# Kernel tuning notes

Measured on AMD Instinct MI355X. Metric: run time of the kernel, lower is better.

## Reference

```python
import jax, jax.numpy as jnp
import numpy as np

B, S, D_IN, D_OUT = 4, 2048, 1024, 1024

def setup_inputs() -> dict:
    key = jax.random.key(0)
    kx, kq, kk, kv = jax.random.split(key, 4)
    x = jax.random.normal(kx, (B, S, D_IN), dtype=jnp.float32)
    # torch nn.Linear weight is [d_out, d_in]; we store the transposed [d_in, d_out]
    # so y = x @ W, scaled like default init to keep magnitudes sane.
    scale = 1.0 / np.sqrt(D_IN)
    Wq = jax.random.normal(kq, (D_IN, D_OUT), dtype=jnp.float32) * scale
    Wk = jax.random.normal(kk, (D_IN, D_OUT), dtype=jnp.float32) * scale
    Wv = jax.random.normal(kv, (D_IN, D_OUT), dtype=jnp.float32) * scale
    return {"x": x, "Wq": Wq, "Wk": Wk, "Wv": Wv}

def reference(x, Wq, Wk, Wv):
    b, n, _ = x.shape
    q = jnp.einsum('bnd,de->bne', x, Wq)   # [B,S,D_OUT]
    k = jnp.einsum('bnd,de->bne', x, Wk)
    v = jnp.einsum('bnd,de->bne', x, Wv)
    scores = jnp.einsum('bqe,bke->bqk', q, k) / jnp.sqrt(jnp.float32(k.shape[-1]))
    causal = jnp.triu(jnp.ones((n, n), dtype=bool), k=1)  # True above diagonal -> masked
    scores = jnp.where(causal[None, :, :], -jnp.inf, scores)
    weights = jax.nn.softmax(scores, axis=-1)
    # dropout p=0.0 (deterministic baseline) -> identity
    context = jnp.einsum('bqk,bke->bqe', weights, v)
    return context
```

## Files before the change

kernel.cpp:

```cpp
#include <hip/hip_runtime.h>
#include <hip/hip_bf16.h>

#define BB 4
#define SS 2048
#define DD 1024

typedef __attribute__((ext_vector_type(8))) short bf16x8;
typedef __attribute__((ext_vector_type(4))) float f32x4;

__device__ __forceinline__ ushort f2bf(float f) {
  unsigned u = __float_as_uint(f);
  unsigned r = (u + 0x7fffu + ((u >> 16) & 1u)) >> 16;
  return (ushort)r;
}

__device__ __forceinline__ void gload_lds16(const void* g, void* l) {
  __builtin_amdgcn_global_load_lds(
      (const __attribute__((address_space(1))) void*)g,
      (__attribute__((address_space(3))) void*)l, 16, 0, 0);
}

__global__ __launch_bounds__(256) void cast_x_kernel(const float* __restrict__ x,
                                                     ushort* __restrict__ xb) {
  const int i = blockIdx.x * 256 + threadIdx.x;
  const float4 a = ((const float4*)x)[2 * i];
  const float4 b = ((const float4*)x)[2 * i + 1];
  ushort4 o0, o1;
  o0.x = f2bf(a.x); o0.y = f2bf(a.y); o0.z = f2bf(a.z); o0.w = f2bf(a.w);
  o1.x = f2bf(b.x); o1.y = f2bf(b.y); o1.z = f2bf(b.z); o1.w = f2bf(b.w);
  ((ushort4*)xb)[2 * i] = o0;
  ((ushort4*)xb)[2 * i + 1] = o1;
}

__global__ __launch_bounds__(256) void cast_transpose_w(const float* __restrict__ W0,
                                                        const float* __restrict__ W1,
                                                        const float* __restrict__ W2,
                                                        ushort* __restrict__ Wt) {
  const float* W = blockIdx.z == 0 ? W0 : (blockIdx.z == 1 ? W1 : W2);
  ushort* O = Wt + (size_t)blockIdx.z * DD * DD;
  __shared__ ushort t[32][33];
  const int n0 = blockIdx.x * 32, k0 = blockIdx.y * 32;
  const int tx = threadIdx.x, ty = threadIdx.y;
#pragma unroll
  for (int j = 0; j < 4; j++) {
    int k = k0 + ty + j * 8;
    t[ty + j * 8][tx] = f2bf(W[(size_t)k * DD + n0 + tx]);
  }
  __syncthreads();
#pragma unroll
  for (int j = 0; j < 4; j++) {
    int n = ty + j * 8;
    O[(size_t)(n0 + n) * DD + k0 + tx] = t[tx][n];
  }
}

template <int BM, int BN, int GMODE, bool EXPMASK, bool KCLIP, bool DIVL, bool OUT_BF16>
__global__ __launch_bounds__(512) void gemm8(const ushort* __restrict__ A, int lda, size_t strA,
                                             const ushort* __restrict__ Bt, int ldb, size_t strB,
                                             void* __restrict__ C, int ldc, size_t strC, int K,
                                             int NBX) {
  constexpr int LA = BM / 64;
  constexpr int LB = BN / 64;
  constexpr int FM = BM / 32;
  constexpr int FN = BN / 64;
  int nb, mb, bz;
  if (GMODE == 2) {
    constexpr int NMB = SS / BM;
    constexpr int T = NMB * (NMB + 1) / 2;
    int flat = blockIdx.x + T * blockIdx.z;
    flat = (flat & 7) * ((T * BB) >> 3) + (flat >> 3);
    bz = flat / T;
    int i = flat % T;
    mb = (int)((sqrtf(8.f * i + 1.f) - 1.f) * 0.5f);
    while ((mb + 1) * (mb + 2) / 2 <= i) ++mb;
    while (mb * (mb + 1) / 2 > i) --mb;
    nb = i - mb * (mb + 1) / 2;
  } else if (GMODE == 1) {
    const int nwg = gridDim.x;
    int L = (blockIdx.x & 7) * (nwg >> 3) + (blockIdx.x >> 3);
    nb = L % NBX;
    mb = L / NBX;
    bz = 0;
  } else if (GMODE == 3) {
    int L = (blockIdx.x & 7) * 64 + (blockIdx.x >> 3);
    nb = L & 7;
    int G = L >> 3;
    bz = G & 3;
    int h = G >> 2;
    mb = (h & 1) ? (15 - (h >> 1)) : (h >> 1);
  } else {
    nb = blockIdx.x; mb = blockIdx.y; bz = blockIdx.z;
  }
  const ushort* Ab = A + (size_t)bz * strA;
  const ushort* Bb = Bt + (size_t)bz * strB;

  __shared__ ushort lds[2][(BM + BN) * 64];

  const int tid = threadIdx.x;
  const int lane = tid & 63;
  const int wid = tid >> 6;
  const int wr = wid >> 2, wc = wid & 3;
  const int fr = lane & 15, qq = lane >> 4;
  const int sx = (fr & 7) << 4;

  int kEnd = KCLIP ? (mb + 1) * BM : K;
  if (kEnd > K) kEnd = K;
  const int NT = kEnd >> 6;

  auto stage = [&](int kt, int buf) {
    ushort* As = &lds[buf][0];
    ushort* Bs = &lds[buf][BM * 64];
    const ushort* ga = Ab + (size_t)mb * BM * lda + kt * 64;
    const ushort* gb = Bb + (size_t)nb * BN * ldb + kt * 64;
#pragma unroll
    for (int j = 0; j < LA; j++) {
      int D = (j * 512 + tid) * 16;
      int r = D >> 7;
      int cb = (D & 127) ^ ((r & 7) << 4);
      gload_lds16(ga + (size_t)r * lda + (cb >> 1), (char*)As + D);
    }
#pragma unroll
    for (int j = 0; j < LB; j++) {
      int D = (j * 512 + tid) * 16;
      int r = D >> 7;
      int cb = (D & 127) ^ ((r & 7) << 4);
      gload_lds16(gb + (size_t)r * ldb + (cb >> 1), (char*)Bs + D);
    }
  };

  stage(0, 0);
  if (NT > 1) stage(1, 1);

  f32x4 acc[FM][FN] = {};
  float lsum[FM];
#pragma unroll
  for (int i = 0; i < FM; i++) lsum[i] = 0.f;

  for (int kt = 0; kt < NT; ++kt) {
    const int cur = kt & 1;
    if (kt < NT - 1) {
      if constexpr (LA + LB == 6) asm volatile("s_waitcnt vmcnt(6)" ::: "memory");
      else if constexpr (LA + LB == 4) asm volatile("s_waitcnt vmcnt(4)" ::: "memory");
      else asm volatile("s_waitcnt vmcnt(0)" ::: "memory");
    } else {
      asm volatile("s_waitcnt vmcnt(0)" ::: "memory");
    }
    __builtin_amdgcn_s_barrier();
    __builtin_amdgcn_sched_barrier(0);

    const char* As = (const char*)&lds[cur][0];
    const char* Bs = (const char*)&lds[cur][BM * 64];
    __builtin_amdgcn_s_setprio(1);
#pragma unroll
    for (int ks = 0; ks < 2; ++ks) {
      const int kb = ks * 64 + qq * 16;
      bf16x8 a[FM], b[FN];
#pragma unroll
      for (int i = 0; i < FM; i++) {
        int r = wr * (BM / 2) + i * 16 + fr;
        a[i] = *(const bf16x8*)(As + r * 128 + (kb ^ sx));
      }
#pragma unroll
      for (int j = 0; j < FN; j++) {
        int r = wc * (BN / 4) + j * 16 + fr;
        b[j] = *(const bf16x8*)(Bs + r * 128 + (kb ^ sx));
      }
      if (DIVL && wc == 0) {
#pragma unroll
        for (int i = 0; i < FM; i++)
#pragma unroll
          for (int e = 0; e < 8; e++)
            lsum[i] += __uint_as_float((unsigned)(unsigned short)a[i][e] << 16);
      }
#pragma unroll
      for (int i = 0; i < FM; i++)
#pragma unroll
        for (int j = 0; j < FN; j++)
          acc[i][j] = __builtin_amdgcn_mfma_f32_16x16x32_bf16(a[i], b[j], acc[i][j], 0, 0, 0);
    }
    __builtin_amdgcn_s_setprio(0);
    __builtin_amdgcn_s_barrier();
    __builtin_amdgcn_sched_barrier(0);
    if (kt + 2 < NT) stage(kt + 2, cur);
  }

  __shared__ float lds_l[2][BM / 2];
  if (DIVL) {
    if (wc == 0) {
#pragma unroll
      for (int i = 0; i < FM; i++) {
        lsum[i] += __shfl_xor(lsum[i], 16);
        lsum[i] += __shfl_xor(lsum[i], 32);
      }
      if (qq == 0) {
#pragma unroll
        for (int i = 0; i < FM; i++) lds_l[wr][i * 16 + fr] = lsum[i];
      }
    }
    __syncthreads();
  }

  const int col0 = nb * BN + wc * (BN / 4) + fr;
  const int row00 = mb * BM + wr * (BM / 2) + qq * 4;
  if (OUT_BF16) {
    ushort* Cb = (ushort*)C + (size_t)bz * strC;
#pragma unroll
    for (int i = 0; i < FM; i++)
#pragma unroll
      for (int rr = 0; rr < 4; rr++) {
        const int row = row00 + i * 16 + rr;
        size_t ro = (size_t)row * ldc;
#pragma unroll
        for (int j = 0; j < FN; j++) {
          float v = acc[i][j][rr];
          if (EXPMASK) {
            v = __expf(v * 0.03125f);
            if (col0 + j * 16 > row) v = 0.f;
          }
          Cb[ro + col0 + j * 16] = f2bf(v);
        }
      }
  } else {
    float* Cb = (float*)C + (size_t)bz * strC;
#pragma unroll
    for (int i = 0; i < FM; i++)
#pragma unroll
      for (int rr = 0; rr < 4; rr++) {
        size_t ro = (size_t)(row00 + i * 16 + rr) * ldc;
        float invl = 1.f;
        if (DIVL) invl = 1.f / lds_l[wr][i * 16 + qq * 4 + rr];
#pragma unroll
        for (int j = 0; j < FN; j++) Cb[ro + col0 + j * 16] = acc[i][j][rr] * invl;
      }
  }
}

extern "C" void kernel_launch(void* const* d_in, const int* in_sizes, int n_in,
                              void* d_out, int out_size, void* d_ws, size_t ws_size,
                              hipStream_t stream) {
  const float* x = (const float*)d_in[0];
  const float* Wq = (const float*)d_in[1];
  const float* Wk = (const float*)d_in[2];
  const float* Wv = (const float*)d_in[3];

  char* ws = (char*)d_ws;
  ushort* xb = (ushort*)(ws);
  ushort* Wt = (ushort*)(ws + 16777216);
  ushort* QK = (ushort*)(ws + 23068672);
  ushort* Vt = (ushort*)(ws + 56623104);
  ushort* P = (ushort*)(ws + 73400320);

  const size_t SD = (size_t)SS * DD;
  const size_t S2 = (size_t)SS * SS;
  const size_t SQ2 = (size_t)SS * 2048;

  cast_x_kernel<<<(BB * SS * DD) / (256 * 8), 256, 0, stream>>>(x, xb);
  cast_transpose_w<<<dim3(DD / 32, DD / 32, 3), dim3(32, 8), 0, stream>>>(Wq, Wk, Wv, Wt);
  gemm8<128, 128, 1, false, false, false, true><<<dim3(1024), 512, 0, stream>>>(
      xb, DD, 0, Wt, DD, 0, QK, 2048, 0, DD, 16);
  gemm8<128, 128, 1, false, false, false, true><<<dim3(512), 512, 0, stream>>>(
      Wt + 2 * DD * DD, DD, 0, xb, DD, 0, Vt, BB * SS, 0, DD, 64);
  gemm8<128, 128, 2, true, false, false, true><<<dim3(136, 1, BB), 512, 0, stream>>>(
      QK, 2048, SQ2, QK + 1024, 2048, SQ2, P, SS, S2, DD, 0);
  gemm8<128, 128, 3, false, true, true, false><<<dim3(512), 512, 0, stream>>>(
      P, SS, S2, Vt, BB * SS, 2048, d_out, DD, SD, SS, 0);

  (void)in_sizes; (void)n_in; (void)out_size; (void)ws_size;
}
```

Baseline: 155.9 us.

## Store intermediate bf16 matrices in tiled 128x64 blocks for contiguous tile loads

```diff
diff --git a/kernel.cpp b/kernel.cpp
--- a/kernel.cpp
+++ b/kernel.cpp
@@ -20,16 +20,24 @@
       (__attribute__((address_space(3))) void*)l, 16, 0, 0);
 }
 
+__device__ __forceinline__ size_t tadr(int row, int col, int ncols) {
+  return (size_t)(row >> 7) * ((size_t)128 * ncols) + (size_t)(col >> 6) * 8192 +
+         (size_t)((row & 127) * 64 + (col & 63));
+}
+
 __global__ __launch_bounds__(256) void cast_x_kernel(const float* __restrict__ x,
                                                      ushort* __restrict__ xb) {
   const int i = blockIdx.x * 256 + threadIdx.x;
+  const int row = i >> 7;
+  const int cb = (i & 127) << 3;
   const float4 a = ((const float4*)x)[2 * i];
   const float4 b = ((const float4*)x)[2 * i + 1];
   ushort4 o0, o1;
   o0.x = f2bf(a.x); o0.y = f2bf(a.y); o0.z = f2bf(a.z); o0.w = f2bf(a.w);
   o1.x = f2bf(b.x); o1.y = f2bf(b.y); o1.z = f2bf(b.z); o1.w = f2bf(b.w);
-  ((ushort4*)xb)[2 * i] = o0;
-  ((ushort4*)xb)[2 * i + 1] = o1;
+  const size_t d = tadr(row, cb, DD);
+  *(ushort4*)(xb + d) = o0;
+  *(ushort4*)(xb + d + 4) = o1;
 }
 
 __global__ __launch_bounds__(256) void cast_transpose_w(const float* __restrict__ W0,
@@ -50,23 +58,18 @@
 #pragma unroll
   for (int j = 0; j < 4; j++) {
     int n = ty + j * 8;
-    O[(size_t)(n0 + n) * DD + k0 + tx] = t[tx][n];
-  }
-}
-
-template <int BM, int BN, int GMODE, bool EXPMASK, bool KCLIP, bool DIVL, bool OUT_BF16>
-__global__ __launch_bounds__(512) void gemm8(const ushort* __restrict__ A, int lda, size_t strA,
-                                             const ushort* __restrict__ Bt, int ldb, size_t strB,
-                                             void* __restrict__ C, int ldc, size_t strC, int K,
-                                             int NBX) {
-  constexpr int LA = BM / 64;
-  constexpr int LB = BN / 64;
-  constexpr int FM = BM / 32;
-  constexpr int FN = BN / 64;
+    O[tadr(n0 + n, k0 + tx, DD)] = t[tx][n];
+  }
+}
+
+template <int GMODE, bool EXPMASK, bool KCLIP, bool DIVL, bool OUTF32>
+__global__ __launch_bounds__(512) void gemm8(const ushort* __restrict__ A, size_t Apanel,
+                                             size_t strA, const ushort* __restrict__ Bt,
+                                             size_t Bpanel, size_t strB, void* __restrict__ C,
+                                             int ldc, size_t strC, int K, int NBX) {
   int nb, mb, bz;
   if (GMODE == 2) {
-    constexpr int NMB = SS / BM;
-    constexpr int T = NMB * (NMB + 1) / 2;
+    constexpr int T = 136;
     int flat = blockIdx.x + T * blockIdx.z;
     flat = (flat & 7) * ((T * BB) >> 3) + (flat >> 3);
     bz = flat / T;
@@ -91,10 +94,10 @@
   } else {
     nb = blockIdx.x; mb = blockIdx.y; bz = blockIdx.z;
   }
-  const ushort* Ab = A + (size_t)bz * strA;
-  const ushort* Bb = Bt + (size_t)bz * strB;
-
-  __shared__ ushort lds[2][(BM + BN) * 64];
+  const ushort* Ab = A + (size_t)bz * strA + (size_t)mb * Apanel;
+  const ushort* Bb = Bt + (size_t)bz * strB + (size_t)nb * Bpanel;
+
+  __shared__ ushort lds[2][256 * 64];
 
   const int tid = threadIdx.x;
   const int lane = tid & 63;
@@ -103,79 +106,70 @@
   const int fr = lane & 15, qq = lane >> 4;
   const int sx = (fr & 7) << 4;
 
-  int kEnd = KCLIP ? (mb + 1) * BM : K;
+  int kEnd = KCLIP ? (mb + 1) * 128 : K;
   if (kEnd > K) kEnd = K;
   const int NT = kEnd >> 6;
 
   auto stage = [&](int kt, int buf) {
-    ushort* As = &lds[buf][0];
-    ushort* Bs = &lds[buf][BM * 64];
-    const ushort* ga = Ab + (size_t)mb * BM * lda + kt * 64;
-    const ushort* gb = Bb + (size_t)nb * BN * ldb + kt * 64;
-#pragma unroll
-    for (int j = 0; j < LA; j++) {
+    const char* ga = (const char*)(Ab + (size_t)kt * 8192);
+    const char* gb = (const char*)(Bb + (size_t)kt * 8192);
+    char* As = (char*)&lds[buf][0];
+    char* Bs = (char*)&lds[buf][128 * 64];
+#pragma unroll
+    for (int j = 0; j < 2; j++) {
       int D = (j * 512 + tid) * 16;
-      int r = D >> 7;
-      int cb = (D & 127) ^ ((r & 7) << 4);
-      gload_lds16(ga + (size_t)r * lda + (cb >> 1), (char*)As + D);
-    }
-#pragma unroll
-    for (int j = 0; j < LB; j++) {
+      int sw = D ^ ((((D >> 7) & 7)) << 4);
+      gload_lds16(ga + sw, As + D);
+    }
+#pragma unroll
+    for (int j = 0; j < 2; j++) {
       int D = (j * 512 + tid) * 16;
-      int r = D >> 7;
-      int cb = (D & 127) ^ ((r & 7) << 4);
-      gload_lds16(gb + (size_t)r * ldb + (cb >> 1), (char*)Bs + D);
+      int sw = D ^ ((((D >> 7) & 7)) << 4);
+      gload_lds16(gb + sw, Bs + D);
     }
   };
 
   stage(0, 0);
   if (NT > 1) stage(1, 1);
 
-  f32x4 acc[FM][FN] = {};
-  float lsum[FM];
-#pragma unroll
-  for (int i = 0; i < FM; i++) lsum[i] = 0.f;
+  f32x4 acc[4][2] = {};
+  float lsum[4] = {0.f, 0.f, 0.f, 0.f};
 
   for (int kt = 0; kt < NT; ++kt) {
     const int cur = kt & 1;
-    if (kt < NT - 1) {
-      if constexpr (LA + LB == 6) asm volatile("s_waitcnt vmcnt(6)" ::: "memory");
-      else if constexpr (LA + LB == 4) asm volatile("s_waitcnt vmcnt(4)" ::: "memory");
-      else asm volatile("s_waitcnt vmcnt(0)" ::: "memory");
-    } else {
-      asm volatile("s_waitcnt vmcnt(0)" ::: "memory");
-    }
+    if (kt < NT - 1) asm volatile("s_waitcnt vmcnt(4)" ::: "memory");
+    else             asm volatile("s_waitcnt vmcnt(0)" ::: "memory");
     __builtin_amdgcn_s_barrier();
     __builtin_amdgcn_sched_barrier(0);
 
     const char* As = (const char*)&lds[cur][0];
-    const char* Bs = (const char*)&lds[cur][BM * 64];
+    const char* Bs = (const char*)&lds[cur][128 * 64];
     __builtin_amdgcn_s_setprio(1);
 #pragma unroll
     for (int ks = 0; ks < 2; ++ks) {
       const int kb = ks * 64 + qq * 16;
-      bf16x8 a[FM], b[FN];
-#pragma unroll
-      for (int i = 0; i < FM; i++) {
-        int r = wr * (BM / 2) + i * 16 + fr;
+      bf16x8 a[4], b[2];
+#pragma unroll
+      for (int i = 0; i < 4; i++) {
+        int r = wr * 64 + i * 16 + fr;
         a[i] = *(const bf16x8*)(As + r * 128 + (kb ^ sx));
       }
 #pragma unroll
-      for (int j = 0; j < FN; j++) {
-        int r = wc * (BN / 4) + j * 16 + fr;
+      for (int j = 0; j < 2; j++) {
+        int r = wc * 32 + j * 16 + fr;
         b[j] = *(const bf16x8*)(Bs + r * 128 + (kb ^ sx));
       }
       if (DIVL && wc == 0) {
 #pragma unroll
-        for (int i = 0; i < FM; i++)
+        for (int i = 0; i < 4; i++)
 #pragma unroll
           for (int e = 0; e < 8; e++)
             lsum[i] += __uint_as_float((unsigned)(unsigned short)a[i][e] << 16);
       }
 #pragma unroll
-      for (int i = 0; i < FM; i++)
-#pragma unroll
-        for (int j = 0; j < FN; j++)
+      for (int i = 0; i < 4; i++)
+#pragma unroll
+        for (int j = 0; j < 2; j++)
           acc[i][j] = __builtin_amdgcn_mfma_f32_16x16x32_bf16(a[i], b[j], acc[i][j], 0, 0, 0);
     }
     __builtin_amdgcn_s_setprio(0);
@@ -184,53 +178,53 @@
     if (kt + 2 < NT) stage(kt + 2, cur);
   }
 
-  __shared__ float lds_l[2][BM / 2];
+  __shared__ float lds_l[2][64];
   if (DIVL) {
     if (wc == 0) {
 #pragma unroll
-      for (int i = 0; i < FM; i++) {
+      for (int i = 0; i < 4; i++) {
         lsum[i] += __shfl_xor(lsum[i], 16);
         lsum[i] += __shfl_xor(lsum[i], 32);
       }
       if (qq == 0) {
 #pragma unroll
-        for (int i = 0; i < FM; i++) lds_l[wr][i * 16 + fr] = lsum[i];
+        for (int i = 0; i < 4; i++) lds_l[wr][i * 16 + fr] = lsum[i];
       }
     }
     __syncthreads();
   }
 
-  const int col0 = nb * BN + wc * (BN / 4) + fr;
-  const int row00 = mb * BM + wr * (BM / 2) + qq * 4;
-  if (OUT_BF16) {
-    ushort* Cb = (ushort*)C + (size_t)bz * strC;
-#pragma unroll
-    for (int i = 0; i < FM; i++)
-#pragma unroll
-      for (int rr = 0; rr < 4; rr++) {
-        const int row = row00 + i * 16 + rr;
-        size_t ro = (size_t)row * ldc;
-#pragma unroll
-        for (int j = 0; j < FN; j++) {
-          float v = acc[i][j][rr];
-          if (EXPMASK) {
-            v = __expf(v * 0.03125f);
-            if (col0 + j * 16 > row) v = 0.f;
-          }
-          Cb[ro + col0 + j * 16] = f2bf(v);
-        }
-      }
-  } else {
+  const int col0 = nb * 128 + wc * 32 + fr;
+  const int row00 = mb * 128 + wr * 64 + qq * 4;
+  if (OUTF32) {
     float* Cb = (float*)C + (size_t)bz * strC;
 #pragma unroll
-    for (int i = 0; i < FM; i++)
+    for (int i = 0; i < 4; i++)
 #pragma unroll
       for (int rr = 0; rr < 4; rr++) {
         size_t ro = (size_t)(row00 + i * 16 + rr) * ldc;
         float invl = 1.f;
         if (DIVL) invl = 1.f / lds_l[wr][i * 16 + qq * 4 + rr];
 #pragma unroll
-        for (int j = 0; j < FN; j++) Cb[ro + col0 + j * 16] = acc[i][j][rr] * invl;
+        for (int j = 0; j < 2; j++) Cb[ro + col0 + j * 16] = acc[i][j][rr] * invl;
+      }
+  } else {
+    ushort* Cb = (ushort*)C + (size_t)bz * strC;
+#pragma unroll
+    for (int i = 0; i < 4; i++)
+#pragma unroll
+      for (int rr = 0; rr < 4; rr++) {
+        const int row = row00 + i * 16 + rr;
+#pragma unroll
+        for (int j = 0; j < 2; j++) {
+          const int col = col0 + j * 16;
+          float v = acc[i][j][rr];
+          if (EXPMASK) {
+            v = __expf(v * 0.03125f);
+            if (col > row) v = 0.f;
+          }
+          Cb[tadr(row, col, ldc)] = f2bf(v);
+        }
       }
   }
 }
@@ -253,17 +247,20 @@
   const size_t SD = (size_t)SS * DD;
   const size_t S2 = (size_t)SS * SS;
   const size_t SQ2 = (size_t)SS * 2048;
+  const size_t PAN_D = (size_t)128 * DD;
+  const size_t PAN_2K = (size_t)128 * 2048;
+  const size_t PAN_8K = (size_t)128 * 8192;
 
   cast_x_kernel<<<(BB * SS * DD) / (256 * 8), 256, 0, stream>>>(x, xb);
   cast_transpose_w<<<dim3(DD / 32, DD / 32, 3), dim3(32, 8), 0, stream>>>(Wq, Wk, Wv, Wt);
-  gemm8<128, 128, 1, false, false, false, true><<<dim3(1024), 512, 0, stream>>>(
-      xb, DD, 0, Wt, DD, 0, QK, 2048, 0, DD, 16);
-  gemm8<128, 128, 1, false, false, false, true><<<dim3(512), 512, 0, stream>>>(
-      Wt + 2 * DD * DD, DD, 0, xb, DD, 0, Vt, BB * SS, 0, DD, 64);
-  gemm8<128, 128, 2, true, false, false, true><<<dim3(136, 1, BB), 512, 0, stream>>>(
-      QK, 2048, SQ2, QK + 1024, 2048, SQ2, P, SS, S2, DD, 0);
-  gemm8<128, 128, 3, false, true, true, false><<<dim3(512), 512, 0, stream>>>(
-      P, SS, S2, Vt, BB * SS, 2048, d_out, DD, SD, SS, 0);
+  gemm8<1, false, false, false, false><<<dim3(1024), 512, 0, stream>>>(
+      xb, PAN_D, 0, Wt, PAN_D, 0, QK, 2048, 0, DD, 16);
+  gemm8<1, false, false, false, false><<<dim3(512), 512, 0, stream>>>(
+      Wt + 2 * DD * DD, PAN_D, 0, xb, PAN_D, 0, Vt, 8192, 0, DD, 64);
+  gemm8<2, true, false, false, false><<<dim3(136, 1, BB), 512, 0, stream>>>(
+      QK, PAN_2K, SQ2, QK + 16 * 8192, PAN_2K, SQ2, P, 2048, S2, DD, 0);
+  gemm8<3, false, true, true, true><<<dim3(512), 512, 0, stream>>>(
+      P, PAN_2K, S2, Vt, PAN_8K, (size_t)32 * 8192, d_out, DD, SD, SS, 0);
 
   (void)in_sizes; (void)n_in; (void)out_size; (void)ws_size;
 }
```

Measured after the change: 158.2 us. Within noise of the previous version (+1.5%).

## Replace PV GEMM with dual-phase 128x64 tile kernel pairing short and long causal rows

Applied to the files above, without the earlier changes.

```diff
diff --git a/kernel.cpp b/kernel.cpp
--- a/kernel.cpp
+++ b/kernel.cpp
@@ -23,13 +23,14 @@
 __global__ __launch_bounds__(256) void cast_x_kernel(const float* __restrict__ x,
                                                      ushort* __restrict__ xb) {
   const int i = blockIdx.x * 256 + threadIdx.x;
-  const float4 a = ((const float4*)x)[2 * i];
-  const float4 b = ((const float4*)x)[2 * i + 1];
-  ushort4 o0, o1;
-  o0.x = f2bf(a.x); o0.y = f2bf(a.y); o0.z = f2bf(a.z); o0.w = f2bf(a.w);
-  o1.x = f2bf(b.x); o1.y = f2bf(b.y); o1.z = f2bf(b.z); o1.w = f2bf(b.w);
-  ((ushort4*)xb)[2 * i] = o0;
-  ((ushort4*)xb)[2 * i + 1] = o1;
+#pragma unroll
+  for (int j = 0; j < 4; j++) {
+    const int idx = i + j * 524288;
+    const float4 a = ((const float4*)x)[idx];
+    ushort4 o;
+    o.x = f2bf(a.x); o.y = f2bf(a.y); o.z = f2bf(a.z); o.w = f2bf(a.w);
+    ((ushort4*)xb)[idx] = o;
+  }
 }
 
 __global__ __launch_bounds__(256) void cast_transpose_w(const float* __restrict__ W0,
@@ -54,7 +55,7 @@
   }
 }
 
-template <int BM, int BN, int GMODE, bool EXPMASK, bool KCLIP, bool DIVL, bool OUT_BF16>
+template <int BM, int BN, int GMODE, bool EXPMASK, bool OUT_BF16>
 __global__ __launch_bounds__(512) void gemm8(const ushort* __restrict__ A, int lda, size_t strA,
                                              const ushort* __restrict__ Bt, int ldb, size_t strB,
                                              void* __restrict__ C, int ldc, size_t strC, int K,
@@ -65,8 +66,7 @@
   constexpr int FN = BN / 64;
   int nb, mb, bz;
   if (GMODE == 2) {
-    constexpr int NMB = SS / BM;
-    constexpr int T = NMB * (NMB + 1) / 2;
+    constexpr int T = 136;
     int flat = blockIdx.x + T * blockIdx.z;
     flat = (flat & 7) * ((T * BB) >> 3) + (flat >> 3);
     bz = flat / T;
@@ -75,21 +75,12 @@
     while ((mb + 1) * (mb + 2) / 2 <= i) ++mb;
     while (mb * (mb + 1) / 2 > i) --mb;
     nb = i - mb * (mb + 1) / 2;
-  } else if (GMODE == 1) {
+  } else {
     const int nwg = gridDim.x;
     int L = (blockIdx.x & 7) * (nwg >> 3) + (blockIdx.x >> 3);
     nb = L % NBX;
     mb = L / NBX;
     bz = 0;
-  } else if (GMODE == 3) {
-    int L = (blockIdx.x & 7) * 64 + (blockIdx.x >> 3);
-    nb = L & 7;
-    int G = L >> 3;
-    bz = G & 3;
-    int h = G >> 2;
-    mb = (h & 1) ? (15 - (h >> 1)) : (h >> 1);
-  } else {
-    nb = blockIdx.x; mb = blockIdx.y; bz = blockIdx.z;
   }
   const ushort* Ab = A + (size_t)bz * strA;
   const ushort* Bb = Bt + (size_t)bz * strB;
@@ -103,9 +94,7 @@
   const int fr = lane & 15, qq = lane >> 4;
   const int sx = (fr & 7) << 4;
 
-  int kEnd = KCLIP ? (mb + 1) * BM : K;
-  if (kEnd > K) kEnd = K;
-  const int NT = kEnd >> 6;
+  const int NT = K >> 6;
 
   auto stage = [&](int kt, int buf) {
     ushort* As = &lds[buf][0];
@@ -132,15 +121,11 @@
   if (NT > 1) stage(1, 1);
 
   f32x4 acc[FM][FN] = {};
-  float lsum[FM];
-#pragma unroll
-  for (int i = 0; i < FM; i++) lsum[i] = 0.f;
 
   for (int kt = 0; kt < NT; ++kt) {
     const int cur = kt & 1;
     if (kt < NT - 1) {
-      if constexpr (LA + LB == 6) asm volatile("s_waitcnt vmcnt(6)" ::: "memory");
-      else if constexpr (LA + LB == 4) asm volatile("s_waitcnt vmcnt(4)" ::: "memory");
+      if constexpr (LA + LB == 4) asm volatile("s_waitcnt vmcnt(4)" ::: "memory");
       else asm volatile("s_waitcnt vmcnt(0)" ::: "memory");
     } else {
       asm volatile("s_waitcnt vmcnt(0)" ::: "memory");
@@ -164,13 +149,6 @@
       for (int j = 0; j < FN; j++) {
         int r = wc * (BN / 4) + j * 16 + fr;
         b[j] = *(const bf16x8*)(Bs + r * 128 + (kb ^ sx));
-      }
-      if (DIVL && wc == 0) {
-#pragma unroll
-        for (int i = 0; i < FM; i++)
-#pragma unroll
-          for (int e = 0; e < 8; e++)
-            lsum[i] += __uint_as_float((unsigned)(unsigned short)a[i][e] << 16);
       }
 #pragma unroll
       for (int i = 0; i < FM; i++)
@@ -182,22 +160,6 @@
     __builtin_amdgcn_s_barrier();
     __builtin_amdgcn_sched_barrier(0);
     if (kt + 2 < NT) stage(kt + 2, cur);
-  }
-
-  __shared__ float lds_l[2][BM / 2];
-  if (DIVL) {
-    if (wc == 0) {
-#pragma unroll
-      for (int i = 0; i < FM; i++) {
-        lsum[i] += __shfl_xor(lsum[i], 16);
-        lsum[i] += __shfl_xor(lsum[i], 32);
-      }
-      if (qq == 0) {
-#pragma unroll
-        for (int i = 0; i < FM; i++) lds_l[wr][i * 16 + fr] = lsum[i];
-      }
-    }
-    __syncthreads();
   }
 
   const int col0 = nb * BN + wc * (BN / 4) + fr;
@@ -227,11 +189,124 @@
 #pragma unroll
       for (int rr = 0; rr < 4; rr++) {
         size_t ro = (size_t)(row00 + i * 16 + rr) * ldc;
-        float invl = 1.f;
-        if (DIVL) invl = 1.f / lds_l[wr][i * 16 + qq * 4 + rr];
-#pragma unroll
-        for (int j = 0; j < FN; j++) Cb[ro + col0 + j * 16] = acc[i][j][rr] * invl;
-      }
+#pragma unroll
+        for (int j = 0; j < FN; j++) Cb[ro + col0 + j * 16] = acc[i][j][rr];
+      }
+  }
+}
+
+__global__ __launch_bounds__(512) void pv_dual(const ushort* __restrict__ P,
+                                               const ushort* __restrict__ Vt,
+                                               float* __restrict__ out) {
+  const int f = blockIdx.x;
+  const int xcd = f & 7, L = f >> 3;
+  const int bz = xcd >> 1, chalf = xcd & 1;
+  const int nd = L & 15, c = chalf * 4 + (L >> 4);
+
+  __shared__ ushort lds[2][(128 + 64) * 64];
+  __shared__ float lds_l[2][64];
+
+  const int tid = threadIdx.x;
+  const int lane = tid & 63, wid = tid >> 6;
+  const int wr = wid >> 2, wc = wid & 3;
+  const int fr = lane & 15, qq = lane >> 4;
+  const int sx = (fr & 7) << 4;
+
+  const ushort* Pb = P + (size_t)bz * SS * SS;
+  const ushort* Bg = Vt + (size_t)bz * 2048 + (size_t)(nd * 64) * 8192;
+
+  auto stageA = [&](int mb, int kt, int buf) {
+    ushort* As = &lds[buf][0];
+    const ushort* ga = Pb + (size_t)(mb * 128) * SS + kt * 64;
+#pragma unroll
+    for (int j = 0; j < 2; j++) {
+      int D = (j * 512 + tid) * 16;
+      int r = D >> 7;
+      int cb = (D & 127) ^ ((r & 7) << 4);
+      gload_lds16(ga + (size_t)r * SS + (cb >> 1), (char*)As + D);
+    }
+  };
+  auto stageB = [&](int kt, int buf) {
+    ushort* Bs = &lds[buf][128 * 64];
+    const ushort* gb = Bg + kt * 64;
+    int D = tid * 16;
+    int r = D >> 7;
+    int cb = (D & 127) ^ ((r & 7) << 4);
+    gload_lds16(gb + (size_t)r * 8192 + (cb >> 1), (char*)Bs + D);
+  };
+
+#pragma unroll 1
+  for (int ph = 0; ph < 2; ++ph) {
+    const int mb = ph == 0 ? c : 15 - c;
+    const int NT = 2 * (mb + 1);
+
+    stageA(mb, 0, 0); stageB(0, 0);
+    if (NT > 1) { stageA(mb, 1, 1); stageB(1, 1); }
+
+    f32x4 acc[4] = {};
+    float lsum[4] = {0.f, 0.f, 0.f, 0.f};
+
+    for (int kt = 0; kt < NT; ++kt) {
+      const int cur = kt & 1;
+      if (kt < NT - 1) asm volatile("s_waitcnt vmcnt(3)" ::: "memory");
+      else             asm volatile("s_waitcnt vmcnt(0)" ::: "memory");
+      __builtin_amdgcn_s_barrier();
+      __builtin_amdgcn_sched_barrier(0);
+
+      const char* As = (const char*)&lds[cur][0];
+      const char* Bs = (const char*)&lds[cur][128 * 64];
+      __builtin_amdgcn_s_setprio(1);
+#pragma unroll
+      for (int ks = 0; ks < 2; ++ks) {
+        const int kb = ks * 64 + qq * 16;
+        bf16x8 a[4], b;
+#pragma unroll
+        for (int i = 0; i < 4; i++) {
+          int r = wr * 64 + i * 16 + fr;
+          a[i] = *(const bf16x8*)(As + r * 128 + (kb ^ sx));
+        }
+        b = *(const bf16x8*)(Bs + (wc * 16 + fr) * 128 + (kb ^ sx));
+        if (wc == 0) {
+#pragma unroll
+          for (int i = 0; i < 4; i++)
+#pragma unroll
+            for (int e = 0; e < 8; e++)
+              lsum[i] += __uint_as_float((unsigned)(unsigned short)a[i][e] << 16);
+        }
+#pragma unroll
+        for (int i = 0; i < 4; i++)
+          acc[i] = __builtin_amdgcn_mfma_f32_16x16x32_bf16(a[i], b, acc[i], 0, 0, 0);
+      }
+      __builtin_amdgcn_s_setprio(0);
+      __builtin_amdgcn_s_barrier();
+      __builtin_amdgcn_sched_barrier(0);
+      if (kt + 2 < NT) { stageA(mb, kt + 2, cur); stageB(kt + 2, cur); }
+    }
+
+    if (wc == 0) {
+#pragma unroll
+      for (int i = 0; i < 4; i++) {
+        lsum[i] += __shfl_xor(lsum[i], 16);
+        lsum[i] += __shfl_xor(lsum[i], 32);
+      }
+      if (qq == 0) {
+#pragma unroll
+        for (int i = 0; i < 4; i++) lds_l[wr][i * 16 + fr] = lsum[i];
+      }
+    }
+    __syncthreads();
+
+    const int col = nd * 64 + wc * 16 + fr;
+    const int row00 = mb * 128 + wr * 64 + qq * 4;
+    float* ob = out + ((size_t)bz * SS) * DD;
+#pragma unroll
+    for (int i = 0; i < 4; i++)
+#pragma unroll
+      for (int rr = 0; rr < 4; rr++) {
+        const float invl = 1.f / lds_l[wr][i * 16 + qq * 4 + rr];
+        ob[(size_t)(row00 + i * 16 + rr) * DD + col] = acc[i][rr] * invl;
+      }
+    __syncthreads();
   }
 }
 
@@ -250,20 +325,18 @@
   ushort* Vt = (ushort*)(ws + 56623104);
   ushort* P = (ushort*)(ws + 73400320);
 
-  const size_t SD = (size_t)SS * DD;
   const size_t S2 = (size_t)SS * SS;
   const size_t SQ2 = (size_t)SS * 2048;
 
-  cast_x_kernel<<<(BB * SS * DD) / (256 * 8), 256, 0, stream>>>(x, xb);
+  cast_x_kernel<<<2048, 256, 0, stream>>>(x, xb);
   cast_transpose_w<<<dim3(DD / 32, DD / 32, 3), dim3(32, 8), 0, stream>>>(Wq, Wk, Wv, Wt);
-  gemm8<128, 128, 1, false, false, false, true><<<dim3(1024), 512, 0, stream>>>(
+  gemm8<128, 128, 1, false, true><<<dim3(1024), 512, 0, stream>>>(
       xb, DD, 0, Wt, DD, 0, QK, 2048, 0, DD, 16);
-  gemm8<128, 128, 1, false, false, false, true><<<dim3(512), 512, 0, stream>>>(
+  gemm8<128, 128, 1, false, true><<<dim3(512), 512, 0, stream>>>(
       Wt + 2 * DD * DD, DD, 0, xb, DD, 0, Vt, BB * SS, 0, DD, 64);
-  gemm8<128, 128, 2, true, false, false, true><<<dim3(136, 1, BB), 512, 0, stream>>>(
+  gemm8<128, 128, 2, true, true><<<dim3(136, 1, BB), 512, 0, stream>>>(
       QK, 2048, SQ2, QK + 1024, 2048, SQ2, P, SS, S2, DD, 0);
-  gemm8<128, 128, 3, false, true, true, false><<<dim3(512), 512, 0, stream>>>(
-      P, SS, S2, Vt, BB * SS, 2048, d_out, DD, SD, SS, 0);
+  pv_dual<<<dim3(512), 512, 0, stream>>>(P, Vt, (float*)d_out);
 
   (void)in_sizes; (void)n_in; (void)out_size; (void)ws_size;
 }
```

After: 159.6 us. 2.4% more time.
